# Kernel tuning notes

Hardware: AMD Instinct MI355X
Metric: run time of the kernel (lower is better)

The kernel has to match this reference:

```python
import jax, jax.numpy as jnp
import numpy as np

N, DEG, D_IN, D_HID = 50000, 16, 963, 256


def setup_inputs() -> dict:
    key = jax.random.key(0)
    ks = jax.random.split(key, 8)
    s = 0.02
    neighbours = jax.random.randint(ks[0], (N, DEG), 0, N)
    shape_features = jax.random.normal(ks[1], (N, D_IN), dtype=jnp.float32)
    # layer 0: D_IN -> D_HID; layers 1..13 (stacked): D_HID -> D_HID; extra: D_HID -> 3
    W_self0 = jax.random.normal(ks[2], (D_IN, D_HID), dtype=jnp.float32) * s
    W_neigh0 = jax.random.normal(ks[3], (D_IN, D_HID), dtype=jnp.float32) * s
    b0 = jnp.zeros((D_HID,), jnp.float32)
    W_self = jax.random.normal(ks[4], (13, D_HID, D_HID), dtype=jnp.float32) * s
    W_neigh = jax.random.normal(ks[5], (13, D_HID, D_HID), dtype=jnp.float32) * s
    b = jnp.zeros((13, D_HID), jnp.float32)
    W_extra = jax.random.normal(ks[6], (D_HID, 3), dtype=jnp.float32) * s
    b_extra = jnp.zeros((3,), jnp.float32)
    return {
        "neighbours": neighbours,
        "shape_features": shape_features,
        "W_self0": W_self0, "W_neigh0": W_neigh0, "b0": b0,
        "W_self": W_self, "W_neigh": W_neigh, "b": b,
        "W_extra": W_extra, "b_extra": b_extra,
    }


def _gcn(x, neighbours, Ws, Wn, bias):
    # gather neighbour features [N, DEG, D] and sum-aggregate, plus self transform
    agg = jnp.take(x, neighbours, axis=0).sum(axis=1)
    return x @ Ws + agg @ Wn + bias


def reference(neighbours, shape_features, W_self0, W_neigh0, b0, W_self, W_neigh, b, W_extra, b_extra):
    x = jax.nn.relu(_gcn(shape_features, neighbours, W_self0, W_neigh0, b0))
    for i in range(6):  # 6 residual blocks of 2 GCN layers each
        temp = x
        x = jax.nn.relu(_gcn(x, neighbours, W_self[2 * i], W_neigh[2 * i], b[2 * i]))
        x = jax.nn.relu(_gcn(x, neighbours, W_self[2 * i + 1], W_neigh[2 * i + 1], b[2 * i + 1]))
        x = (temp + x) / 2
    x = jax.nn.relu(_gcn(x, neighbours, W_self[12], W_neigh[12], b[12]))
    coordinates = x @ W_extra + b_extra  # extra layer called without neighbours -> linear
    return (x, coordinates)
```

## Files before the change

kernel.cpp:

```cpp
#include <hip/hip_runtime.h>
#include <hip/hip_bf16.h>
#include <hip/hip_fp16.h>
#include <stdint.h>

#define NNODES 50000
#define NPAD   50048
#define DEG    16
#define DIN    963
#define K0PAD  992
#define DHID   256
#define SCALE  (1.0f / 1024.0f)
#define ISCALE 1024.0f

typedef __attribute__((ext_vector_type(4))) float    f32x4;
typedef __attribute__((ext_vector_type(8))) _Float16 f16x8;
typedef __attribute__((ext_vector_type(4))) _Float16 f16x4;

typedef const __attribute__((address_space(1))) void GV;
typedef __attribute__((address_space(3))) void LV;

__device__ __forceinline__ void gl2lds16(const void* g, void* l) {
    __builtin_amdgcn_global_load_lds((GV*)g, (LV*)l, 16, 0, 0);
}

__global__ __launch_bounds__(512) void gemm_mfma(
    const _Float16* __restrict__ A, int K,
    const _Float16* __restrict__ Wp,
    _Float16* __restrict__ ys, _Float16* __restrict__ yn)
{
    __shared__ _Float16 ldsA[2][4096];
    __shared__ _Float16 ldsB[2][8192];

    const int tid  = threadIdx.x;
    const int w    = tid >> 6;
    const int lane = tid & 63;

    const int nwg = gridDim.x;
    const int bid = blockIdx.x;
    const int q = nwg >> 3, r = nwg & 7, xc = bid & 7;
    const int wgid = (xc < r ? xc * (q + 1) : r * (q + 1) + (xc - r) * q) + (bid >> 3);
    const int bm = (wgid >> 1) << 7;
    const int by = wgid & 1;
    const int nb = by << 8;

    const int KT = K >> 5;

    auto stage = [&](int s, int kt) {
        const int k0 = kt << 5;
        {
            const int c = (w << 6) + lane;
            gl2lds16(A + (size_t)(bm + (c & 127)) * K + k0 + ((c >> 7) << 3),
                     &ldsA[s][(size_t)w << 9]);
        }
#pragma unroll
        for (int i = 0; i < 2; ++i) {
            const int j = w + (i << 3);
            const int c = (j << 6) + lane;
            gl2lds16(Wp + (size_t)(nb + (c & 255)) * K + k0 + ((c >> 8) << 3),
                     &ldsB[s][(size_t)j << 9]);
        }
    };

    const int wm = (w >> 2) << 6;
    const int wn = (w & 3) << 6;
    const int lr = lane & 15;
    const int kh = lane >> 4;

    f32x4 acc[4][4] = {};

    stage(0, 0);
    __syncthreads();
    int cur = 0;
    for (int kt = 0; kt < KT; ++kt) {
        if (kt + 1 < KT) stage(cur ^ 1, kt + 1);
        f16x8 a[4], b[4];
#pragma unroll
        for (int mi = 0; mi < 4; ++mi)
            a[mi] = *(const f16x8*)&ldsA[cur][((kh << 7) + wm + (mi << 4) + lr) << 3];
#pragma unroll
        for (int ni = 0; ni < 4; ++ni)
            b[ni] = *(const f16x8*)&ldsB[cur][((kh << 8) + wn + (ni << 4) + lr) << 3];
#pragma unroll
        for (int mi = 0; mi < 4; ++mi)
#pragma unroll
            for (int ni = 0; ni < 4; ++ni)
                acc[mi][ni] = __builtin_amdgcn_mfma_f32_16x16x32_f16(a[mi], b[ni], acc[mi][ni], 0, 0, 0);
        __syncthreads();
        cur ^= 1;
    }

    _Float16* C = (by == 0) ? ys : yn;
#pragma unroll
    for (int mi = 0; mi < 4; ++mi) {
        const size_t rbase = (size_t)(bm + wm + (mi << 4) + (kh << 2)) << 8;
#pragma unroll
        for (int ni = 0; ni < 4; ++ni) {
            const int col = wn + (ni << 4) + lr;
#pragma unroll
            for (int r = 0; r < 4; ++r)
                C[rbase + ((size_t)r << 8) + col] = (_Float16)acc[mi][ni][r];
        }
    }
}

__global__ __launch_bounds__(256) void combine(
    const _Float16* __restrict__ ys, const _Float16* __restrict__ yn,
    const int* __restrict__ nbr, const float* __restrict__ bias,
    const _Float16* __restrict__ res,
    _Float16* __restrict__ outh, float* __restrict__ outf)
{
    const int w    = threadIdx.x >> 6;
    const int lane = threadIdx.x & 63;
    const int n    = (blockIdx.x << 2) + w;
    const int c4   = lane << 2;
    const size_t base = ((size_t)n << 8) + c4;

    const f16x4 ysv = *(const f16x4*)(ys + base);
    const float4 bv = *(const float4*)(bias + c4);
    float s0 = (float)ysv[0] + bv.x * SCALE;
    float s1 = (float)ysv[1] + bv.y * SCALE;
    float s2 = (float)ysv[2] + bv.z * SCALE;
    float s3 = (float)ysv[3] + bv.w * SCALE;

    const int* nr = nbr + n * DEG;
#pragma unroll
    for (int j = 0; j < DEG; ++j) {
        const f16x4 v = *(const f16x4*)(yn + (((size_t)nr[j]) << 8) + c4);
        s0 += (float)v[0]; s1 += (float)v[1]; s2 += (float)v[2]; s3 += (float)v[3];
    }
    s0 = fmaxf(s0, 0.f); s1 = fmaxf(s1, 0.f); s2 = fmaxf(s2, 0.f); s3 = fmaxf(s3, 0.f);
    if (res) {
        const f16x4 rv = *(const f16x4*)(res + base);
        s0 = ((float)rv[0] + s0) * 0.5f;
        s1 = ((float)rv[1] + s1) * 0.5f;
        s2 = ((float)rv[2] + s2) * 0.5f;
        s3 = ((float)rv[3] + s3) * 0.5f;
    }
    if (outh) {
        f16x4 o;
        o[0] = (_Float16)s0; o[1] = (_Float16)s1; o[2] = (_Float16)s2; o[3] = (_Float16)s3;
        *(f16x4*)(outh + base) = o;
    } else {
        float4 o = make_float4(s0 * ISCALE, s1 * ISCALE, s2 * ISCALE, s3 * ISCALE);
        *(float4*)(outf + base) = o;
    }
}

__global__ __launch_bounds__(64) void coords_kernel(
    const float* __restrict__ x, const float* __restrict__ We,
    const float* __restrict__ be, float* __restrict__ out3, int N)
{
    const int n = blockIdx.x;
    const int l = threadIdx.x;
    const float4 xv = *(const float4*)(x + (size_t)n * 256 + l * 4);
    float p0 = 0.f, p1 = 0.f, p2 = 0.f;
    const float xs[4] = {xv.x, xv.y, xv.z, xv.w};
#pragma unroll
    for (int i = 0; i < 4; ++i) {
        const int cidx = l * 4 + i;
        p0 += xs[i] * We[cidx * 3 + 0];
        p1 += xs[i] * We[cidx * 3 + 1];
        p2 += xs[i] * We[cidx * 3 + 2];
    }
#pragma unroll
    for (int off = 32; off > 0; off >>= 1) {
        p0 += __shfl_down(p0, off);
        p1 += __shfl_down(p1, off);
        p2 += __shfl_down(p2, off);
    }
    if (l == 0) {
        out3[(size_t)n * 3 + 0] = p0 + be[0];
        out3[(size_t)n * 3 + 1] = p1 + be[1];
        out3[(size_t)n * 3 + 2] = p2 + be[2];
    }
}

__global__ __launch_bounds__(256) void conv_sf(const float* __restrict__ sf,
                                               _Float16* __restrict__ sfb)
{
    const int idx = blockIdx.x * 256 + threadIdx.x;
    const int row = idx / 124;
    const int k8  = (idx % 124) << 3;
    f16x8 o = {};
    if (row < NNODES) {
#pragma unroll
        for (int i = 0; i < 8; ++i) {
            const int k = k8 + i;
            o[i] = (k < DIN) ? (_Float16)(sf[(size_t)row * DIN + k] * SCALE) : (_Float16)0.f;
        }
    }
    *(f16x8*)(sfb + (size_t)row * K0PAD + k8) = o;
}

__global__ __launch_bounds__(256) void pack_w0(const float* __restrict__ Ws0,
                                               const float* __restrict__ Wn0,
                                               _Float16* __restrict__ Wp0)
{
    const int idx = blockIdx.x * 256 + threadIdx.x;
    const int nn  = idx & 511;
    const int k8  = idx >> 9;
    const float* W = (nn < 256) ? Ws0 : Wn0;
    const int n0 = nn & 255;
    f16x8 o;
#pragma unroll
    for (int i = 0; i < 8; ++i) {
        const int k = (k8 << 3) + i;
        o[i] = (k < DIN) ? (_Float16)W[(size_t)k * 256 + n0] : (_Float16)0.f;
    }
    *(f16x8*)(Wp0 + (size_t)nn * K0PAD + (k8 << 3)) = o;
}

__global__ __launch_bounds__(256) void pack_w(const float* __restrict__ Ws,
                                              const float* __restrict__ Wn,
                                              _Float16* __restrict__ Wpk)
{
    const int idx = blockIdx.x * 256 + threadIdx.x;
    const int nn  = idx & 511;
    const int k8  = (idx >> 9) & 31;
    const int l   = idx >> 14;
    const float* W = (nn < 256) ? Ws : Wn;
    const int n0 = nn & 255;
    f16x8 o;
#pragma unroll
    for (int i = 0; i < 8; ++i)
        o[i] = (_Float16)W[(size_t)l * 65536 + ((k8 << 3) + i) * 256 + n0];
    *(f16x8*)(Wpk + (size_t)l * 131072 + (size_t)nn * 256 + (k8 << 3)) = o;
}

extern "C" void kernel_launch(void* const* d_in, const int* in_sizes, int n_in,
                              void* d_out, int out_size, void* d_ws, size_t ws_size,
                              hipStream_t stream)
{
    const int*   nbr = (const int*)d_in[0];
    const float* sf  = (const float*)d_in[1];
    const float* Ws0 = (const float*)d_in[2];
    const float* Wn0 = (const float*)d_in[3];
    const float* b0  = (const float*)d_in[4];
    const float* Ws  = (const float*)d_in[5];
    const float* Wn  = (const float*)d_in[6];
    const float* bb  = (const float*)d_in[7];
    const float* We  = (const float*)d_in[8];
    const float* be  = (const float*)d_in[9];
    float* out = (float*)d_out;

    uint8_t* w = (uint8_t*)d_ws;
    _Float16* sfb = (_Float16*)w;
    _Float16* P   = (_Float16*)w;
    _Float16* Q   = P + (size_t)NPAD * 256;
    _Float16* Wpk = Q + (size_t)NPAD * 256;
    _Float16* Wp0 = (_Float16*)(w + (size_t)NPAD * K0PAD * 2);
    _Float16* ysb = Wp0 + (size_t)512 * K0PAD;
    _Float16* ynb = ysb + (size_t)NPAD * 256;

    conv_sf<<<NPAD * 124 / 256, 256, 0, stream>>>(sf, sfb);
    pack_w0<<<512 * 124 / 256, 256, 0, stream>>>(Ws0, Wn0, Wp0);

    const int gemmGrid = (NPAD / 128) * 2;

    gemm_mfma<<<gemmGrid, 512, 0, stream>>>(sfb, K0PAD, Wp0, ysb, ynb);
    pack_w<<<13 * 512 * 32 / 256, 256, 0, stream>>>(Ws, Wn, Wpk);
    combine<<<NNODES / 4, 256, 0, stream>>>(ysb, ynb, nbr, b0, nullptr, P, nullptr);

    for (int t = 0; t < 6; ++t) {
        const int lA = 2 * t, lB = lA + 1;
        gemm_mfma<<<gemmGrid, 512, 0, stream>>>(P, 256, Wpk + (size_t)lA * 131072, ysb, ynb);
        combine<<<NNODES / 4, 256, 0, stream>>>(ysb, ynb, nbr, bb + lA * 256, nullptr, Q, nullptr);
        gemm_mfma<<<gemmGrid, 512, 0, stream>>>(Q, 256, Wpk + (size_t)lB * 131072, ysb, ynb);
        combine<<<NNODES / 4, 256, 0, stream>>>(ysb, ynb, nbr, bb + lB * 256, P, P, nullptr);
    }

    gemm_mfma<<<gemmGrid, 512, 0, stream>>>(P, 256, Wpk + (size_t)12 * 131072, ysb, ynb);
    combine<<<NNODES / 4, 256, 0, stream>>>(ysb, ynb, nbr, bb + 12 * 256, nullptr, nullptr, out);

    coords_kernel<<<NNODES, 64, 0, stream>>>(out, We, be, out + (size_t)NNODES * 256, NNODES);
}
```

Baseline: 1.599 ms.

## Aggregate neighbours first, then run one fused K=512 GEMM with epilogue

For the 13 hidden layers, neighbour features are now summed first by a dedicated gather kernel. A single GEMM then runs over the concatenated [x, agg] input against stacked [Ws; Wn] weights, with bias, ReLU, residual averaging and output conversion fused into its epilogue. This removes the separate ys/yn intermediate writes and the combine pass that re-read them, at the cost of an extra agg buffer round trip and a 64-row tile with a 512-deep K loop. The first layer GEMM is also retiled to 128x128 blocks on a 2D grid with 256 threads.

```diff
diff --git a/kernel.cpp b/kernel.cpp
--- a/kernel.cpp
+++ b/kernel.cpp
@@ -23,46 +23,36 @@
     __builtin_amdgcn_global_load_lds((GV*)g, (LV*)l, 16, 0, 0);
 }
 
-__global__ __launch_bounds__(512) void gemm_mfma(
+__global__ __launch_bounds__(256) void gemm_dual0(
     const _Float16* __restrict__ A, int K,
     const _Float16* __restrict__ Wp,
     _Float16* __restrict__ ys, _Float16* __restrict__ yn)
 {
-    __shared__ _Float16 ldsA[2][4096];
-    __shared__ _Float16 ldsB[2][8192];
+    __shared__ _Float16 lds[2][2][4096];
 
     const int tid  = threadIdx.x;
     const int w    = tid >> 6;
     const int lane = tid & 63;
-
-    const int nwg = gridDim.x;
-    const int bid = blockIdx.x;
-    const int q = nwg >> 3, r = nwg & 7, xc = bid & 7;
-    const int wgid = (xc < r ? xc * (q + 1) : r * (q + 1) + (xc - r) * q) + (bid >> 3);
-    const int bm = (wgid >> 1) << 7;
-    const int by = wgid & 1;
-    const int nb = by << 8;
+    const int bm   = blockIdx.x * 128;
+    const int nb   = blockIdx.y * 128;
 
     const int KT = K >> 5;
 
     auto stage = [&](int s, int kt) {
         const int k0 = kt << 5;
-        {
-            const int c = (w << 6) + lane;
-            gl2lds16(A + (size_t)(bm + (c & 127)) * K + k0 + ((c >> 7) << 3),
-                     &ldsA[s][(size_t)w << 9]);
-        }
 #pragma unroll
         for (int i = 0; i < 2; ++i) {
-            const int j = w + (i << 3);
-            const int c = (j << 6) + lane;
-            gl2lds16(Wp + (size_t)(nb + (c & 255)) * K + k0 + ((c >> 8) << 3),
-                     &ldsB[s][(size_t)j << 9]);
+            const int j   = w + (i << 2);
+            const int c   = (j << 6) + lane;
+            const int row = c & 127;
+            const int k8  = (c >> 7) << 3;
+            gl2lds16(A  + (size_t)(bm + row) * K + k0 + k8, &lds[s][0][(size_t)j << 9]);
+            gl2lds16(Wp + (size_t)(nb + row) * K + k0 + k8, &lds[s][1][(size_t)j << 9]);
         }
     };
 
-    const int wm = (w >> 2) << 6;
-    const int wn = (w & 3) << 6;
+    const int wm = (w >> 1) << 6;
+    const int wn = (w & 1) << 6;
     const int lr = lane & 15;
     const int kh = lane >> 4;
 
@@ -76,10 +66,10 @@
         f16x8 a[4], b[4];
 #pragma unroll
         for (int mi = 0; mi < 4; ++mi)
-            a[mi] = *(const f16x8*)&ldsA[cur][((kh << 7) + wm + (mi << 4) + lr) << 3];
+            a[mi] = *(const f16x8*)&lds[cur][0][((kh << 7) + wm + (mi << 4) + lr) << 3];
 #pragma unroll
         for (int ni = 0; ni < 4; ++ni)
-            b[ni] = *(const f16x8*)&ldsB[cur][((kh << 8) + wn + (ni << 4) + lr) << 3];
+            b[ni] = *(const f16x8*)&lds[cur][1][((kh << 7) + wn + (ni << 4) + lr) << 3];
 #pragma unroll
         for (int mi = 0; mi < 4; ++mi)
 #pragma unroll
@@ -89,13 +79,14 @@
         cur ^= 1;
     }
 
-    _Float16* C = (by == 0) ? ys : yn;
+    _Float16* C = (blockIdx.y < 2) ? ys : yn;
+    const int cb = (nb & 255) + wn;
 #pragma unroll
     for (int mi = 0; mi < 4; ++mi) {
         const size_t rbase = (size_t)(bm + wm + (mi << 4) + (kh << 2)) << 8;
 #pragma unroll
         for (int ni = 0; ni < 4; ++ni) {
-            const int col = wn + (ni << 4) + lr;
+            const int col = cb + (ni << 4) + lr;
 #pragma unroll
             for (int r = 0; r < 4; ++r)
                 C[rbase + ((size_t)r << 8) + col] = (_Float16)acc[mi][ni][r];
@@ -103,11 +94,118 @@
     }
 }
 
-__global__ __launch_bounds__(256) void combine(
+template<int FINAL>
+__global__ __launch_bounds__(256) void gemm_fused(
+    const _Float16* __restrict__ X, const _Float16* __restrict__ AG,
+    const _Float16* __restrict__ W, const float* __restrict__ bias,
+    const _Float16* __restrict__ res,
+    _Float16* __restrict__ outh, float* __restrict__ outf)
+{
+    __shared__ _Float16 ldsA[2][2048];
+    __shared__ _Float16 ldsB[2][8192];
+
+    const int tid  = threadIdx.x;
+    const int w    = tid >> 6;
+    const int lane = tid & 63;
+
+    const int nwg = gridDim.x, bid = blockIdx.x;
+    const int q = nwg >> 3, r_ = nwg & 7, xc = bid & 7;
+    const int wgid = (xc < r_ ? xc * (q + 1) : r_ * (q + 1) + (xc - r_) * q) + (bid >> 3);
+    const int bm = wgid << 6;
+
+    auto stage = [&](int s, int kt) {
+        const _Float16* src = (kt < 8) ? X : AG;
+        const int kl = (kt & 7) << 5;
+        {
+            const int c = tid;
+            gl2lds16(src + (size_t)(bm + (c & 63)) * 256 + kl + ((c >> 6) << 3),
+                     &ldsA[s][(size_t)w << 9]);
+        }
+#pragma unroll
+        for (int i = 0; i < 4; ++i) {
+            const int j = (i << 2) + w;
+            const int c = (j << 6) + lane;
+            gl2lds16(W + (size_t)(c & 255) * 512 + (kt << 5) + ((c >> 8) << 3),
+                     &ldsB[s][(size_t)j << 9]);
+        }
+    };
+
+    const int wn = w << 6;
+    const int lr = lane & 15;
+    const int k4 = lane >> 4;
+
+    f32x4 acc[4][4] = {};
+
+    stage(0, 0);
+    __syncthreads();
+    int cur = 0;
+    for (int kt = 0; kt < 16; ++kt) {
+        if (kt + 1 < 16) stage(cur ^ 1, kt + 1);
+        f16x8 a[4], b[4];
+#pragma unroll
+        for (int mi = 0; mi < 4; ++mi)
+            a[mi] = *(const f16x8*)&ldsA[cur][((k4 << 6) + (mi << 4) + lr) << 3];
+#pragma unroll
+        for (int ni = 0; ni < 4; ++ni)
+            b[ni] = *(const f16x8*)&ldsB[cur][((k4 << 8) + wn + (ni << 4) + lr) << 3];
+#pragma unroll
+        for (int mi = 0; mi < 4; ++mi)
+#pragma unroll
+            for (int ni = 0; ni < 4; ++ni)
+                acc[mi][ni] = __builtin_amdgcn_mfma_f32_16x16x32_f16(a[mi], b[ni], acc[mi][ni], 0, 0, 0);
+        __syncthreads();
+        cur ^= 1;
+    }
+
+    const int r0 = k4 << 2;
+#pragma unroll
+    for (int mi = 0; mi < 4; ++mi) {
+        const int grow0 = bm + (mi << 4) + r0;
+#pragma unroll
+        for (int ni = 0; ni < 4; ++ni) {
+            const int col = wn + (ni << 4) + lr;
+            const float bcol = bias[col] * SCALE;
+#pragma unroll
+            for (int r = 0; r < 4; ++r) {
+                const int grow = grow0 + r;
+                float s = acc[mi][ni][r] + bcol;
+                s = fmaxf(s, 0.f);
+                if (res) s = ((float)res[((size_t)grow << 8) + col] + s) * 0.5f;
+                if (FINAL) {
+                    if (grow < NNODES) outf[((size_t)grow << 8) + col] = s * ISCALE;
+                } else {
+                    outh[((size_t)grow << 8) + col] = (_Float16)s;
+                }
+            }
+        }
+    }
+}
+
+__global__ __launch_bounds__(256) void gather_sum(
+    const _Float16* __restrict__ x, const int* __restrict__ nbr,
+    _Float16* __restrict__ agg)
+{
+    const int w    = threadIdx.x >> 6;
+    const int lane = threadIdx.x & 63;
+    const int n    = (blockIdx.x << 2) + w;
+    const int c4   = lane << 2;
+
+    const int* nr = nbr + n * DEG;
+    float s0 = 0.f, s1 = 0.f, s2 = 0.f, s3 = 0.f;
+#pragma unroll
+    for (int j = 0; j < DEG; ++j) {
+        const f16x4 v = *(const f16x4*)(x + (((size_t)nr[j]) << 8) + c4);
+        s0 += (float)v[0]; s1 += (float)v[1]; s2 += (float)v[2]; s3 += (float)v[3];
+    }
+    f16x4 o;
+    o[0] = (_Float16)s0; o[1] = (_Float16)s1; o[2] = (_Float16)s2; o[3] = (_Float16)s3;
+    *(f16x4*)(agg + (((size_t)n) << 8) + c4) = o;
+}
+
+__global__ __launch_bounds__(256) void combine0(
     const _Float16* __restrict__ ys, const _Float16* __restrict__ yn,
     const int* __restrict__ nbr, const float* __restrict__ bias,
-    const _Float16* __restrict__ res,
-    _Float16* __restrict__ outh, float* __restrict__ outf)
+    _Float16* __restrict__ outh)
 {
     const int w    = threadIdx.x >> 6;
     const int lane = threadIdx.x & 63;
@@ -128,22 +226,10 @@
         const f16x4 v = *(const f16x4*)(yn + (((size_t)nr[j]) << 8) + c4);
         s0 += (float)v[0]; s1 += (float)v[1]; s2 += (float)v[2]; s3 += (float)v[3];
     }
-    s0 = fmaxf(s0, 0.f); s1 = fmaxf(s1, 0.f); s2 = fmaxf(s2, 0.f); s3 = fmaxf(s3, 0.f);
-    if (res) {
-        const f16x4 rv = *(const f16x4*)(res + base);
-        s0 = ((float)rv[0] + s0) * 0.5f;
-        s1 = ((float)rv[1] + s1) * 0.5f;
-        s2 = ((float)rv[2] + s2) * 0.5f;
-        s3 = ((float)rv[3] + s3) * 0.5f;
-    }
-    if (outh) {
-        f16x4 o;
-        o[0] = (_Float16)s0; o[1] = (_Float16)s1; o[2] = (_Float16)s2; o[3] = (_Float16)s3;
-        *(f16x4*)(outh + base) = o;
-    } else {
-        float4 o = make_float4(s0 * ISCALE, s1 * ISCALE, s2 * ISCALE, s3 * ISCALE);
-        *(float4*)(outf + base) = o;
-    }
+    f16x4 o;
+    o[0] = (_Float16)fmaxf(s0, 0.f); o[1] = (_Float16)fmaxf(s1, 0.f);
+    o[2] = (_Float16)fmaxf(s2, 0.f); o[3] = (_Float16)fmaxf(s3, 0.f);
+    *(f16x4*)(outh + base) = o;
 }
 
 __global__ __launch_bounds__(64) void coords_kernel(
@@ -210,21 +296,22 @@
     *(f16x8*)(Wp0 + (size_t)nn * K0PAD + (k8 << 3)) = o;
 }
 
-__global__ __launch_bounds__(256) void pack_w(const float* __restrict__ Ws,
-                                              const float* __restrict__ Wn,
-                                              _Float16* __restrict__ Wpk)
+__global__ __launch_bounds__(256) void pack_w2(const float* __restrict__ Ws,
+                                               const float* __restrict__ Wn,
+                                               _Float16* __restrict__ Wpk2)
 {
     const int idx = blockIdx.x * 256 + threadIdx.x;
-    const int nn  = idx & 511;
-    const int k8  = (idx >> 9) & 31;
+    const int n   = idx & 255;
+    const int k8  = (idx >> 8) & 63;
     const int l   = idx >> 14;
-    const float* W = (nn < 256) ? Ws : Wn;
-    const int n0 = nn & 255;
     f16x8 o;
 #pragma unroll
-    for (int i = 0; i < 8; ++i)
-        o[i] = (_Float16)W[(size_t)l * 65536 + ((k8 << 3) + i) * 256 + n0];
-    *(f16x8*)(Wpk + (size_t)l * 131072 + (size_t)nn * 256 + (k8 << 3)) = o;
+    for (int i = 0; i < 8; ++i) {
+        const int k = (k8 << 3) + i;
+        const float* W = (k < 256) ? Ws : Wn;
+        o[i] = (_Float16)W[(size_t)l * 65536 + (k & 255) * 256 + n];
+    }
+    *(f16x8*)(Wpk2 + (size_t)l * 131072 + (size_t)n * 512 + (k8 << 3)) = o;
 }
 
 extern "C" void kernel_launch(void* const* d_in, const int* in_sizes, int n_in,
@@ -244,33 +331,37 @@
     float* out = (float*)d_out;
 
     uint8_t* w = (uint8_t*)d_ws;
-    _Float16* sfb = (_Float16*)w;
-    _Float16* P   = (_Float16*)w;
-    _Float16* Q   = P + (size_t)NPAD * 256;
-    _Float16* Wpk = Q + (size_t)NPAD * 256;
-    _Float16* Wp0 = (_Float16*)(w + (size_t)NPAD * K0PAD * 2);
-    _Float16* ysb = Wp0 + (size_t)512 * K0PAD;
-    _Float16* ynb = ysb + (size_t)NPAD * 256;
+    _Float16* sfb  = (_Float16*)w;
+    _Float16* P    = (_Float16*)w;
+    _Float16* Q    = P + (size_t)NPAD * 256;
+    _Float16* Wpk2 = Q + (size_t)NPAD * 256;
+    _Float16* Wp0  = (_Float16*)(w + (size_t)NPAD * K0PAD * 2);
+    _Float16* ysb  = Wp0 + (size_t)512 * K0PAD;
+    _Float16* ynb  = ysb + (size_t)NPAD * 256;
+    _Float16* agg  = ysb;
 
     conv_sf<<<NPAD * 124 / 256, 256, 0, stream>>>(sf, sfb);
     pack_w0<<<512 * 124 / 256, 256, 0, stream>>>(Ws0, Wn0, Wp0);
 
-    const int gemmGrid = (NPAD / 128) * 2;
-
-    gemm_mfma<<<gemmGrid, 512, 0, stream>>>(sfb, K0PAD, Wp0, ysb, ynb);
-    pack_w<<<13 * 512 * 32 / 256, 256, 0, stream>>>(Ws, Wn, Wpk);
-    combine<<<NNODES / 4, 256, 0, stream>>>(ysb, ynb, nbr, b0, nullptr, P, nullptr);
+    gemm_dual0<<<dim3(NPAD / 128, 4), 256, 0, stream>>>(sfb, K0PAD, Wp0, ysb, ynb);
+    pack_w2<<<13 * 64 * 256 / 256, 256, 0, stream>>>(Ws, Wn, Wpk2);
+    combine0<<<NNODES / 4, 256, 0, stream>>>(ysb, ynb, nbr, b0, P);
+
+    const int fg = NPAD / 64;
 
     for (int t = 0; t < 6; ++t) {
         const int lA = 2 * t, lB = lA + 1;
-        gemm_mfma<<<gemmGrid, 512, 0, stream>>>(P, 256, Wpk + (size_t)lA * 131072, ysb, ynb);
-        combine<<<NNODES / 4, 256, 0, stream>>>(ysb, ynb, nbr, bb + lA * 256, nullptr, Q, nullptr);
-        gemm_mfma<<<gemmGrid, 512, 0, stream>>>(Q, 256, Wpk + (size_t)lB * 131072, ysb, ynb);
-        combine<<<NNODES / 4, 256, 0, stream>>>(ysb, ynb, nbr, bb + lB * 256, P, P, nullptr);
-    }
-
-    gemm_mfma<<<gemmGrid, 512, 0, stream>>>(P, 256, Wpk + (size_t)12 * 131072, ysb, ynb);
-    combine<<<NNODES / 4, 256, 0, stream>>>(ysb, ynb, nbr, bb + 12 * 256, nullptr, nullptr, out);
+        gather_sum<<<NNODES / 4, 256, 0, stream>>>(P, nbr, agg);
+        gemm_fused<0><<<fg, 256, 0, stream>>>(P, agg, Wpk2 + (size_t)lA * 131072,
+                                              bb + lA * 256, nullptr, Q, nullptr);
+        gather_sum<<<NNODES / 4, 256, 0, stream>>>(Q, nbr, agg);
+        gemm_fused<0><<<fg, 256, 0, stream>>>(Q, agg, Wpk2 + (size_t)lB * 131072,
+                                              bb + lB * 256, P, P, nullptr);
+    }
+
+    gather_sum<<<NNODES / 4, 256, 0, stream>>>(P, nbr, agg);
+    gemm_fused<1><<<fg, 256, 0, stream>>>(P, agg, Wpk2 + (size_t)12 * 131072,
+                                          bb + 12 * 256, nullptr, nullptr, out);
 
     coords_kernel<<<NNODES, 64, 0, stream>>>(out, We, be, out + (size_t)NNODES * 256, NNODES);
 }
```

Measured after the change: 1.826 ms. 1.14x slower.
